# Performance work log

Hardware: AMD Instinct MI355X
Metric: run time of the kernel (lower is better)

The kernel has to match this reference:

```python
import jax, jax.numpy as jnp
import numpy as np
import math

B, S, H = 8, 1024, 1024
NH, DH = 16, 64  # MULTI_HEAD, HIDDEN_SIZE_HEAD


def setup_inputs() -> dict:
    key = jax.random.key(0)
    ks = jax.random.split(key, 12)
    scale = 0.02
    inp = {
        "v": jax.random.normal(ks[0], (B, S, H), jnp.float32),
        "k": jax.random.normal(ks[1], (B, S, H), jnp.float32),
        "q": jax.random.normal(ks[2], (B, S, H), jnp.float32),
        # True = masked position (masked_fill semantics)
        "mask": jax.random.bernoulli(ks[3], 0.1, (B, 1, 1, S)),
        "Wq": jax.random.normal(ks[4], (H, H), jnp.float32) * scale,
        "bq": jnp.zeros((H,), jnp.float32),
        "Wk": jax.random.normal(ks[5], (H, H), jnp.float32) * scale,
        "bk": jnp.zeros((H,), jnp.float32),
        "Wv": jax.random.normal(ks[6], (H, H), jnp.float32) * scale,
        "bv": jnp.zeros((H,), jnp.float32),
        "Wm": jax.random.normal(ks[7], (H, H), jnp.float32) * scale,
        "bm": jnp.zeros((H,), jnp.float32),
    }
    return inp


def _split_heads(x):
    # [B, S, H] -> [B, NH, S, DH]
    b, s, _ = x.shape
    return x.reshape(b, s, NH, DH).transpose(0, 2, 1, 3)


def reference(v, k, q, mask, Wq, bq, Wk, bk, Wv, bv, Wm, bm):
    # QKV projections (torch Linear: x @ W.T + b)
    qh = _split_heads(q @ Wq.T + bq)  # [B, NH, S, DH]
    kh = _split_heads(k @ Wk.T + bk)
    vh = _split_heads(v @ Wv.T + bv)

    scores = jnp.einsum("bhqd,bhkd->bhqk", qh, kh) / math.sqrt(DH)
    scores = jnp.where(mask, jnp.float32(-1e9), scores)
    att = jax.nn.softmax(scores, axis=-1)
    # dropout rate 0.0 (eval mode) -> identity
    ctx = jnp.einsum("bhqk,bhkd->bhqd", att, vh)  # [B, NH, S, DH]

    b = q.shape[0]
    merged = ctx.transpose(0, 2, 1, 3).reshape(b, -1, NH * DH)  # [B, S, H]
    return merged @ Wm.T + bm
```

## Files before the change

### kernel.cpp

```cpp
#include <hip/hip_runtime.h>
#include <hip/hip_bf16.h>

#define Bn 8
#define Sn 1024
#define Hn 1024
#define NHn 16
#define DHn 64
#define Mn (Bn * Sn)

typedef unsigned short u16;
typedef short bf16x8 __attribute__((ext_vector_type(8)));
typedef unsigned short u16x4 __attribute__((ext_vector_type(4)));
typedef float f32x4 __attribute__((ext_vector_type(4)));

__device__ __forceinline__ u16 f2bf(float x) {
  union { __hip_bfloat16 h; u16 u; } cv;
  cv.h = __float2bfloat16(x);
  return cv.u;
}

__device__ __forceinline__ void async_ld16(void* lds, const void* g) {
  __builtin_amdgcn_global_load_lds(
      (const __attribute__((address_space(1))) void*)g,
      (__attribute__((address_space(3))) void*)lds, 16, 0, 0);
}


__global__ __launch_bounds__(256) void sniff_k(const void* __restrict__ mask,
                                               int* __restrict__ flags) {
  __shared__ int viol;
  if (threadIdx.x == 0) viol = 0;
  __syncthreads();
  const unsigned* mw = (const unsigned*)mask;
  int vb = 0;
#pragma unroll
  for (int j = 0; j < 8; ++j) {
    unsigned v = mw[threadIdx.x * 8 + j];
    if (v > 1u) vb |= 1;
    if ((v & 0xFEFEFEFEu) != 0u) vb |= 2;
    if (!(v == 0u || v == 0x3F800000u)) vb |= 4;
    unsigned h0 = v & 0xFFFFu, h1 = v >> 16;
    if (!((h0 == 0u || h0 == 0x3F80u) && (h1 == 0u || h1 == 0x3F80u))) vb |= 8;
  }
  if (vb) atomicOr(&viol, vb);
  __syncthreads();
  if (threadIdx.x == 0) {
    int mt;
    if (!(viol & 1))      mt = 0;
    else if (!(viol & 2)) mt = 1;
    else if (!(viol & 4)) mt = 3;
    else if (!(viol & 8)) mt = 2;
    else                  mt = 0;
    flags[1] = mt;
  }
}

__global__ __launch_bounds__(256) void convert3(
    const float* __restrict__ a, const float* __restrict__ b,
    const float* __restrict__ c, u16* __restrict__ da,
    u16* __restrict__ db, u16* __restrict__ dc) {
  const int seg = blockIdx.x >> 12;
  const int bid = blockIdx.x & 4095;
  const float* s = seg == 0 ? a : seg == 1 ? b : c;
  u16* d        = seg == 0 ? da : seg == 1 ? db : dc;
  const int i = (bid * 256 + threadIdx.x) * 8;
  f32x4 lo = *(const f32x4*)(s + i);
  f32x4 hi = *(const f32x4*)(s + i + 4);
  bf16x8 o;
#pragma unroll
  for (int j = 0; j < 4; ++j) { o[j] = (short)f2bf(lo[j]); o[4 + j] = (short)f2bf(hi[j]); }
  *(bf16x8*)(d + i) = o;
}

__global__ __launch_bounds__(256) void convertW(
    const float* __restrict__ a, const float* __restrict__ b,
    const float* __restrict__ c, const float* __restrict__ e,
    u16* __restrict__ da, u16* __restrict__ db,
    u16* __restrict__ dc, u16* __restrict__ de) {
  const int seg = blockIdx.x >> 9;
  const int bid = blockIdx.x & 511;
  const float* s = seg == 0 ? a : seg == 1 ? b : seg == 2 ? c : e;
  u16* d        = seg == 0 ? da : seg == 1 ? db : seg == 2 ? dc : de;
  const int i = (bid * 256 + threadIdx.x) * 8;
  f32x4 lo = *(const f32x4*)(s + i);
  f32x4 hi = *(const f32x4*)(s + i + 4);
  bf16x8 o;
#pragma unroll
  for (int j = 0; j < 4; ++j) { o[j] = (short)f2bf(lo[j]); o[4 + j] = (short)f2bf(hi[j]); }
  *(bf16x8*)(d + i) = o;
}

template <int OMODE>
__device__ __forceinline__ void gemm_core(
    u16* As, u16* Bs, const u16* __restrict__ X, const u16* __restrict__ W,
    const float* __restrict__ bias, void* __restrict__ O, float scale)
{
  const int tid  = threadIdx.x;
  const int wave = tid >> 6;
  const int lane = tid & 63;
  const int ln   = lane & 15;
  const int quad = lane >> 4;
  const int bxr  = blockIdx.x;
  const int m0 = ((bxr & 7) * 8 + (bxr >> 3)) * 128;
  const int n0 = blockIdx.y * 128;
  const int wm = (wave & 1) * 64;
  const int wn = (wave >> 1) * 64;
  const int r8 = tid >> 3;
  const int cg = ((tid & 7) ^ (r8 & 7)) * 8;
  const int rsw = ln & 7;

  f32x4 acc[4][4] = {};

  auto STAGE = [&](int buf, int k0) {
    char* Ad = (char*)As + buf * 16384 + wave * 1024;
    char* Bd = (char*)Bs + buf * 16384 + wave * 1024;
#pragma unroll
    for (int j = 0; j < 4; ++j) {
      async_ld16(Ad + j * 4096, X + (size_t)(m0 + j * 32 + r8) * 1024 + k0 + cg);
      async_ld16(Bd + j * 4096, W + (size_t)(n0 + j * 32 + r8) * 1024 + k0 + cg);
    }
  };

  STAGE(0, 0);
  for (int step = 0; step < 16; ++step) {
    const int cur = step & 1;
    if (step < 15) {
      STAGE(cur ^ 1, (step + 1) * 64);
      asm volatile("s_waitcnt vmcnt(8)" ::: "memory");
    } else {
      asm volatile("s_waitcnt vmcnt(0)" ::: "memory");
    }
    asm volatile("s_barrier" ::: "memory");
    const char* Ab = (const char*)As + cur * 16384;
    const char* Bb = (const char*)Bs + cur * 16384;
#pragma unroll
    for (int s = 0; s < 2; ++s) {
      const int co = ((s * 4 + quad) ^ rsw) * 16;
      bf16x8 af[4], bfr[4];
#pragma unroll
      for (int t = 0; t < 4; ++t)
        af[t] = *(const bf16x8*)(Ab + (wm + t * 16 + ln) * 128 + co);
#pragma unroll
      for (int t = 0; t < 4; ++t)
        bfr[t] = *(const bf16x8*)(Bb + (wn + t * 16 + ln) * 128 + co);
#pragma unroll
      for (int i = 0; i < 4; ++i)
#pragma unroll
        for (int j = 0; j < 4; ++j)
          acc[i][j] = __builtin_amdgcn_mfma_f32_16x16x32_bf16(af[i], bfr[j], acc[i][j], 0, 0, 0);
    }
    asm volatile("s_barrier" ::: "memory");
  }

  if (OMODE == 2) {
    const int bb = m0 >> 10;
    const int sb = m0 & 1023;
#pragma unroll
    for (int j = 0; j < 4; ++j) {
      const int col = n0 + wn + j * 16 + ln;
      const float bv = bias[col];
#pragma unroll
      for (int i = 0; i < 4; ++i) {
        const int sl = sb + wm + i * 16 + quad * 4;
        u16x4 pk;
#pragma unroll
        for (int r = 0; r < 4; ++r) pk[r] = f2bf((acc[i][j][r] + bv) * scale);
        *(u16x4*)&((u16*)O)[((size_t)(bb * 1024 + col)) * 1024 + sl] = pk;
      }
    }
  } else {
#pragma unroll
    for (int j = 0; j < 4; ++j) {
      const int col = n0 + wn + j * 16 + ln;
      const float bv = bias[col];
#pragma unroll
      for (int i = 0; i < 4; ++i) {
        const int rowb = m0 + wm + i * 16 + quad * 4;
#pragma unroll
        for (int r = 0; r < 4; ++r) {
          const float val = (acc[i][j][r] + bv) * scale;
          const size_t idx = (size_t)(rowb + r) * 1024 + col;
          if (OMODE == 1) ((float*)O)[idx] = val;
          else            ((u16*)O)[idx]   = f2bf(val);
        }
      }
    }
  }
}

template <int OMODE>
__global__ __launch_bounds__(256, 2) void gemm_bt(
    const u16* __restrict__ X, const u16* __restrict__ W,
    const float* __restrict__ bias, void* __restrict__ O, float scale)
{
  __shared__ __attribute__((aligned(16))) u16 As[2 * 128 * 64];
  __shared__ __attribute__((aligned(16))) u16 Bs[2 * 128 * 64];
  gemm_core<OMODE>(As, Bs, X, W, bias, O, scale);
}

__global__ __launch_bounds__(256, 2) void gemm_qk(
    const u16* __restrict__ Xq, const u16* __restrict__ Wq,
    const float* __restrict__ bq, u16* __restrict__ Oq,
    const u16* __restrict__ Xk, const u16* __restrict__ Wk,
    const float* __restrict__ bk, u16* __restrict__ Ok)
{
  __shared__ __attribute__((aligned(16))) u16 As[2 * 128 * 64];
  __shared__ __attribute__((aligned(16))) u16 Bs[2 * 128 * 64];
  const int z = blockIdx.z;
  gemm_core<0>(As, Bs, z ? Xk : Xq, z ? Wk : Wq, z ? bk : bq,
               z ? (void*)Ok : (void*)Oq, z ? 1.0f : 0.125f);
}

__global__ __launch_bounds__(256, 3) void attn(
    const u16* __restrict__ Qb, const u16* __restrict__ Kb,
    const u16* __restrict__ Vbt, const void* __restrict__ mask,
    const int* __restrict__ flags, u16* __restrict__ Ctx)
{
  __shared__ __attribute__((aligned(16))) u16 Ks[128 * 64];
  __shared__ __attribute__((aligned(16))) u16 Vt[64 * 128];
  __shared__ __attribute__((aligned(16))) u16 Pl[4][16 * 128];
  __shared__ __attribute__((aligned(16))) float maskf[Sn];

  const int tid  = threadIdx.x;
  const int wave = tid >> 6;
  const int lane = tid & 63;
  const int ln   = lane & 15;
  const int quad = lane >> 4;
  const int bx  = blockIdx.x;
  const int x   = bx & 7;
  const int qt  = (bx >> 3) & 15;
  const int grp = bx >> 7;
  const int bh  = grp * 8 + x;
  const int b   = bh >> 4;
  const int h   = bh & 15;

  const int mt = flags[1];
  for (int i = tid; i < Sn; i += 256) {
    const int idx = b * Sn + i;
    int nz;
    if (mt == 0)      nz = ((const int*)mask)[idx] != 0;
    else if (mt == 1) nz = ((const signed char*)mask)[idx] != 0;
    else if (mt == 2) nz = ((const u16*)mask)[idx] != 0;
    else              nz = ((const unsigned*)mask)[idx] != 0;
    maskf[i] = nz ? -1e9f : 0.0f;
  }

  const size_t qoff = (size_t)(b * Sn + qt * 64 + wave * 16 + ln) * Hn + h * DHn;
  bf16x8 qf0 = *(const bf16x8*)&Qb[qoff + quad * 8];
  bf16x8 qf1 = *(const bf16x8*)&Qb[qoff + 32 + quad * 8];

  float mrun = -INFINITY, lrun = 0.0f;
  f32x4 acc[4] = {};

  const int kr = tid >> 1, kh = tid & 1;
  const int vd = tid >> 2, vs = tid & 3;
  char* pw  = (char*)Pl[wave];
  char* KsB = (char*)Ks;
  char* VtB = (char*)Vt;

  const int kwb = kr * 128 + kh * 64;
  const int ksw = (kr & 7) << 4;
  const int vwb = vd * 256 + vs * 64;
  const int vsw = (vd & 7) << 4;
  const int rsw = (ln & 7) << 4;
  const int pwb = ln * 256;
  const int psw = (ln & 7) << 4;

  const u16* kg = &Kb[(size_t)(b * Sn + kr) * Hn + h * DHn + kh * 32];
  const u16* vg = &Vbt[(size_t)(b * Sn + h * DHn + vd) * Sn + vs * 32];
  bf16x8 kreg[4], vreg[4];
#pragma unroll
  for (int j = 0; j < 4; ++j) kreg[j] = *(const bf16x8*)(kg + j * 8);
#pragma unroll
  for (int j = 0; j < 4; ++j) vreg[j] = *(const bf16x8*)(vg + j * 8);

  for (int t8 = 0; t8 < 8; ++t8) {
    const int kv0 = t8 * 128;
    __syncthreads();
#pragma unroll
    for (int j = 0; j < 4; ++j)
      *(bf16x8*)(KsB + ((kwb + j * 16) ^ ksw)) = kreg[j];
#pragma unroll
    for (int j = 0; j < 4; ++j)
      *(bf16x8*)(VtB + ((vwb + j * 16) ^ vsw)) = vreg[j];
    __syncthreads();

    if (t8 < 7) {
      const u16* kgn = kg + (size_t)(t8 + 1) * 128 * Hn;
      const u16* vgn = vg + (t8 + 1) * 128;
#pragma unroll
      for (int j = 0; j < 4; ++j) kreg[j] = *(const bf16x8*)(kgn + j * 8);
#pragma unroll
      for (int j = 0; j < 4; ++j) vreg[j] = *(const bf16x8*)(vgn + j * 8);
    }

    f32x4 sc[8];
#pragma unroll
    for (int t = 0; t < 8; ++t) {
      const int rb = (t * 16 + ln) * 128;
      bf16x8 kf0 = *(const bf16x8*)(KsB + ((rb + quad * 16) ^ rsw));
      bf16x8 kf1 = *(const bf16x8*)(KsB + ((rb + 64 + quad * 16) ^ rsw));
      f32x4 z = {};
      z = __builtin_amdgcn_mfma_f32_16x16x32_bf16(kf0, qf0, z, 0, 0, 0);
      z = __builtin_amdgcn_mfma_f32_16x16x32_bf16(kf1, qf1, z, 0, 0, 0);
      sc[t] = z;
    }
#pragma unroll
    for (int t = 0; t < 8; ++t) {
      const f32x4 mf4 = *(const f32x4*)&maskf[kv0 + t * 16 + quad * 4];
#pragma unroll
      for (int r = 0; r < 4; ++r) sc[t][r] += mf4[r];
    }

    f32x4 mm = sc[0];
#pragma unroll
    for (int t = 1; t < 8; ++t)
#pragma unroll
      for (int r = 0; r < 4; ++r) mm[r] = fmaxf(mm[r], sc[t][r]);
    float vmax = fmaxf(fmaxf(mm[0], mm[1]), fmaxf(mm[2], mm[3]));
    vmax = fmaxf(vmax, __shfl_xor(vmax, 16));
    vmax = fmaxf(vmax, __shfl_xor(vmax, 32));
    const float mnew = fmaxf(mrun, vmax);
    const float al = __expf(mrun - mnew);
    mrun = mnew;
    float ssum = 0.0f;
#pragma unroll
    for (int t = 0; t < 8; ++t)
#pragma unroll
      for (int r = 0; r < 4; ++r) {
        const float p = __expf(sc[t][r] - mnew);
        sc[t][r] = p;
        ssum += p;
      }
    ssum += __shfl_xor(ssum, 16);
    ssum += __shfl_xor(ssum, 32);
    lrun = lrun * al + ssum;

#pragma unroll
    for (int t = 0; t < 8; ++t) {
      u16x4 pk;
#pragma unroll
      for (int r = 0; r < 4; ++r) pk[r] = f2bf(sc[t][r]);
      *(u16x4*)(pw + ((pwb + t * 32 + quad * 8) ^ psw)) = pk;
    }

    float alr[4];
#pragma unroll
    for (int r = 0; r < 4; ++r) alr[r] = __shfl(al, quad * 4 + r);
#pragma unroll
    for (int dt = 0; dt < 4; ++dt)
#pragma unroll
      for (int r = 0; r < 4; ++r) acc[dt][r] *= alr[r];

    bf16x8 pa[4];
#pragma unroll
    for (int c = 0; c < 4; ++c)
      pa[c] = *(const bf16x8*)(pw + ((pwb + c * 64 + quad * 16) ^ psw));
#pragma unroll
    for (int dt = 0; dt < 4; ++dt) {
      const int vrb = (dt * 16 + ln) * 256;
#pragma unroll
      for (int c = 0; c < 4; ++c) {
        bf16x8 vb = *(const bf16x8*)(VtB + ((vrb + c * 64 + quad * 16) ^ rsw));
        acc[dt] = __builtin_amdgcn_mfma_f32_16x16x32_bf16(pa[c], vb, acc[dt], 0, 0, 0);
      }
    }
  }

  float lr[4];
#pragma unroll
  for (int r = 0; r < 4; ++r) lr[r] = __shfl(lrun, quad * 4 + r);
#pragma unroll
  for (int dt = 0; dt < 4; ++dt)
#pragma unroll
    for (int r = 0; r < 4; ++r) {
      const int s = qt * 64 + wave * 16 + quad * 4 + r;
      Ctx[(size_t)(b * Sn + s) * Hn + h * DHn + dt * 16 + ln] = f2bf(acc[dt][r] / lr[r]);
    }
}

extern "C" void kernel_launch(void* const* d_in, const int* in_sizes, int n_in,
                              void* d_out, int out_size, void* d_ws, size_t ws_size,
                              hipStream_t stream) {
  const float* v    = (const float*)d_in[0];
  const float* k    = (const float*)d_in[1];
  const float* q    = (const float*)d_in[2];
  const void*  mask = d_in[3];
  const float* Wq   = (const float*)d_in[4];
  const float* bq   = (const float*)d_in[5];
  const float* Wk   = (const float*)d_in[6];
  const float* bk   = (const float*)d_in[7];
  const float* Wv   = (const float*)d_in[8];
  const float* bv   = (const float*)d_in[9];
  const float* Wm   = (const float*)d_in[10];
  const float* bm   = (const float*)d_in[11];

  char* ws = (char*)d_ws;
  u16* qc  = (u16*)(ws);
  u16* kc  = (u16*)(ws + (16u << 20));
  u16* vc  = (u16*)(ws + (32u << 20));
  u16* Wqc = (u16*)(ws + (48u << 20));
  u16* Wkc = Wqc + (1u << 20);
  u16* Wvc = Wkc + (1u << 20);
  u16* Wmc = Wvc + (1u << 20);
  int* flags = (int*)(ws + (56u << 20));
  u16* Vbt = qc;
  u16* Cx  = kc;
  u16* Qb  = (u16*)d_out;
  u16* Kb  = Qb + (size_t)Mn * Hn;

  sniff_k<<<1, 256, 0, stream>>>(mask, flags);
  convert3<<<3 * 4096, 256, 0, stream>>>(q, k, v, qc, kc, vc);
  convertW<<<4 * 512, 256, 0, stream>>>(Wq, Wk, Wv, Wm, Wqc, Wkc, Wvc, Wmc);

  dim3 blk(256);
  gemm_qk<<<dim3(Mn / 128, Hn / 128, 2), blk, 0, stream>>>(
      qc, Wqc, bq, Qb, kc, Wkc, bk, Kb);
  dim3 grid(Mn / 128, Hn / 128);
  gemm_bt<2><<<grid, blk, 0, stream>>>(vc, Wvc, bv, Vbt, 1.0f);
  attn<<<dim3(Bn * NHn * (Sn / 64)), blk, 0, stream>>>(Qb, Kb, Vbt, mask, flags, Cx);
  gemm_bt<1><<<grid, blk, 0, stream>>>(Cx, Wmc, bm, d_out, 1.0f);
}
```

Before: 330.9 us.

## Process two 64-row query tiles per attention block to reuse K/V tiles

The attention kernel now handles 128 query rows per block: each wave keeps two 16-row query fragments (A and B) with separate online-softmax state and accumulators. Each K/V tile staged in LDS is reused for twice the query work, halving K/V global traffic and block count. The cost is higher register pressure (launch bounds lowered from 3 to 2 blocks per CU), a larger P buffer in LDS, and fewer blocks for load balancing.

```diff
diff --git a/kernel.cpp b/kernel.cpp
--- a/kernel.cpp
+++ b/kernel.cpp
@@ -24,7 +24,6 @@
       (const __attribute__((address_space(1))) void*)g,
       (__attribute__((address_space(3))) void*)lds, 16, 0, 0);
 }
-
 
 __global__ __launch_bounds__(256) void sniff_k(const void* __restrict__ mask,
                                                int* __restrict__ flags) {
@@ -211,14 +210,14 @@
                z ? (void*)Ok : (void*)Oq, z ? 1.0f : 0.125f);
 }
 
-__global__ __launch_bounds__(256, 3) void attn(
+__global__ __launch_bounds__(256, 2) void attn(
     const u16* __restrict__ Qb, const u16* __restrict__ Kb,
     const u16* __restrict__ Vbt, const void* __restrict__ mask,
     const int* __restrict__ flags, u16* __restrict__ Ctx)
 {
   __shared__ __attribute__((aligned(16))) u16 Ks[128 * 64];
   __shared__ __attribute__((aligned(16))) u16 Vt[64 * 128];
-  __shared__ __attribute__((aligned(16))) u16 Pl[4][16 * 128];
+  __shared__ __attribute__((aligned(16))) u16 Pl[4][32 * 128];
   __shared__ __attribute__((aligned(16))) float maskf[Sn];
 
   const int tid  = threadIdx.x;
@@ -228,8 +227,8 @@
   const int quad = lane >> 4;
   const int bx  = blockIdx.x;
   const int x   = bx & 7;
-  const int qt  = (bx >> 3) & 15;
-  const int grp = bx >> 7;
+  const int qt  = (bx >> 3) & 7;
+  const int grp = bx >> 6;
   const int bh  = grp * 8 + x;
   const int b   = bh >> 4;
   const int h   = bh & 15;
@@ -245,12 +244,16 @@
     maskf[i] = nz ? -1e9f : 0.0f;
   }
 
-  const size_t qoff = (size_t)(b * Sn + qt * 64 + wave * 16 + ln) * Hn + h * DHn;
-  bf16x8 qf0 = *(const bf16x8*)&Qb[qoff + quad * 8];
-  bf16x8 qf1 = *(const bf16x8*)&Qb[qoff + 32 + quad * 8];
-
-  float mrun = -INFINITY, lrun = 0.0f;
-  f32x4 acc[4] = {};
+  const size_t qoffA = (size_t)(b * Sn + qt * 128 + wave * 16 + ln) * Hn + h * DHn;
+  const size_t qoffB = qoffA + (size_t)64 * Hn;
+  bf16x8 qfA0 = *(const bf16x8*)&Qb[qoffA + quad * 8];
+  bf16x8 qfA1 = *(const bf16x8*)&Qb[qoffA + 32 + quad * 8];
+  bf16x8 qfB0 = *(const bf16x8*)&Qb[qoffB + quad * 8];
+  bf16x8 qfB1 = *(const bf16x8*)&Qb[qoffB + 32 + quad * 8];
+
+  float mrunA = -INFINITY, lrunA = 0.0f;
+  float mrunB = -INFINITY, lrunB = 0.0f;
+  f32x4 accA[4] = {}, accB[4] = {};
 
   const int kr = tid >> 1, kh = tid & 1;
   const int vd = tid >> 2, vs = tid & 3;
@@ -263,7 +266,8 @@
   const int vwb = vd * 256 + vs * 64;
   const int vsw = (vd & 7) << 4;
   const int rsw = (ln & 7) << 4;
-  const int pwb = ln * 256;
+  const int pwbA = ln * 256;
+  const int pwbB = (16 + ln) * 256;
   const int psw = (ln & 7) << 4;
 
   const u16* kg = &Kb[(size_t)(b * Sn + kr) * Hn + h * DHn + kh * 32];
@@ -294,88 +298,130 @@
       for (int j = 0; j < 4; ++j) vreg[j] = *(const bf16x8*)(vgn + j * 8);
     }
 
-    f32x4 sc[8];
+    f32x4 scA[8], scB[8];
 #pragma unroll
     for (int t = 0; t < 8; ++t) {
       const int rb = (t * 16 + ln) * 128;
       bf16x8 kf0 = *(const bf16x8*)(KsB + ((rb + quad * 16) ^ rsw));
       bf16x8 kf1 = *(const bf16x8*)(KsB + ((rb + 64 + quad * 16) ^ rsw));
-      f32x4 z = {};
-      z = __builtin_amdgcn_mfma_f32_16x16x32_bf16(kf0, qf0, z, 0, 0, 0);
-      z = __builtin_amdgcn_mfma_f32_16x16x32_bf16(kf1, qf1, z, 0, 0, 0);
-      sc[t] = z;
+      f32x4 zA = {}, zB = {};
+      zA = __builtin_amdgcn_mfma_f32_16x16x32_bf16(kf0, qfA0, zA, 0, 0, 0);
+      zA = __builtin_amdgcn_mfma_f32_16x16x32_bf16(kf1, qfA1, zA, 0, 0, 0);
+      zB = __builtin_amdgcn_mfma_f32_16x16x32_bf16(kf0, qfB0, zB, 0, 0, 0);
+      zB = __builtin_amdgcn_mfma_f32_16x16x32_bf16(kf1, qfB1, zB, 0, 0, 0);
+      scA[t] = zA;
+      scB[t] = zB;
     }
 #pragma unroll
     for (int t = 0; t < 8; ++t) {
       const f32x4 mf4 = *(const f32x4*)&maskf[kv0 + t * 16 + quad * 4];
 #pragma unroll
-      for (int r = 0; r < 4; ++r) sc[t][r] += mf4[r];
-    }
-
-    f32x4 mm = sc[0];
-#pragma unroll
-    for (int t = 1; t < 8; ++t)
-#pragma unroll
-      for (int r = 0; r < 4; ++r) mm[r] = fmaxf(mm[r], sc[t][r]);
-    float vmax = fmaxf(fmaxf(mm[0], mm[1]), fmaxf(mm[2], mm[3]));
-    vmax = fmaxf(vmax, __shfl_xor(vmax, 16));
-    vmax = fmaxf(vmax, __shfl_xor(vmax, 32));
-    const float mnew = fmaxf(mrun, vmax);
-    const float al = __expf(mrun - mnew);
-    mrun = mnew;
-    float ssum = 0.0f;
-#pragma unroll
-    for (int t = 0; t < 8; ++t)
-#pragma unroll
-      for (int r = 0; r < 4; ++r) {
-        const float p = __expf(sc[t][r] - mnew);
-        sc[t][r] = p;
-        ssum += p;
-      }
-    ssum += __shfl_xor(ssum, 16);
-    ssum += __shfl_xor(ssum, 32);
-    lrun = lrun * al + ssum;
+      for (int r = 0; r < 4; ++r) { scA[t][r] += mf4[r]; scB[t][r] += mf4[r]; }
+    }
+
+    float alA, alB;
+    {
+      f32x4 mm = scA[0];
+#pragma unroll
+      for (int t = 1; t < 8; ++t)
+#pragma unroll
+        for (int r = 0; r < 4; ++r) mm[r] = fmaxf(mm[r], scA[t][r]);
+      float vmax = fmaxf(fmaxf(mm[0], mm[1]), fmaxf(mm[2], mm[3]));
+      vmax = fmaxf(vmax, __shfl_xor(vmax, 16));
+      vmax = fmaxf(vmax, __shfl_xor(vmax, 32));
+      const float mnew = fmaxf(mrunA, vmax);
+      alA = __expf(mrunA - mnew);
+      mrunA = mnew;
+      float ssum = 0.0f;
+#pragma unroll
+      for (int t = 0; t < 8; ++t)
+#pragma unroll
+        for (int r = 0; r < 4; ++r) {
+          const float p = __expf(scA[t][r] - mnew);
+          scA[t][r] = p;
+          ssum += p;
+        }
+      ssum += __shfl_xor(ssum, 16);
+      ssum += __shfl_xor(ssum, 32);
+      lrunA = lrunA * alA + ssum;
+    }
+    {
+      f32x4 mm = scB[0];
+#pragma unroll
+      for (int t = 1; t < 8; ++t)
+#pragma unroll
+        for (int r = 0; r < 4; ++r) mm[r] = fmaxf(mm[r], scB[t][r]);
+      float vmax = fmaxf(fmaxf(mm[0], mm[1]), fmaxf(mm[2], mm[3]));
+      vmax = fmaxf(vmax, __shfl_xor(vmax, 16));
+      vmax = fmaxf(vmax, __shfl_xor(vmax, 32));
+      const float mnew = fmaxf(mrunB, vmax);
+      alB = __expf(mrunB - mnew);
+      mrunB = mnew;
+      float ssum = 0.0f;
+#pragma unroll
+      for (int t = 0; t < 8; ++t)
+#pragma unroll
+        for (int r = 0; r < 4; ++r) {
+          const float p = __expf(scB[t][r] - mnew);
+          scB[t][r] = p;
+          ssum += p;
+        }
+      ssum += __shfl_xor(ssum, 16);
+      ssum += __shfl_xor(ssum, 32);
+      lrunB = lrunB * alB + ssum;
+    }
 
 #pragma unroll
     for (int t = 0; t < 8; ++t) {
-      u16x4 pk;
-#pragma unroll
-      for (int r = 0; r < 4; ++r) pk[r] = f2bf(sc[t][r]);
-      *(u16x4*)(pw + ((pwb + t * 32 + quad * 8) ^ psw)) = pk;
-    }
-
-    float alr[4];
-#pragma unroll
-    for (int r = 0; r < 4; ++r) alr[r] = __shfl(al, quad * 4 + r);
+      u16x4 pkA, pkB;
+#pragma unroll
+      for (int r = 0; r < 4; ++r) { pkA[r] = f2bf(scA[t][r]); pkB[r] = f2bf(scB[t][r]); }
+      *(u16x4*)(pw + ((pwbA + t * 32 + quad * 8) ^ psw)) = pkA;
+      *(u16x4*)(pw + ((pwbB + t * 32 + quad * 8) ^ psw)) = pkB;
+    }
+
+    float alrA[4], alrB[4];
+#pragma unroll
+    for (int r = 0; r < 4; ++r) {
+      alrA[r] = __shfl(alA, quad * 4 + r);
+      alrB[r] = __shfl(alB, quad * 4 + r);
+    }
 #pragma unroll
     for (int dt = 0; dt < 4; ++dt)
 #pragma unroll
-      for (int r = 0; r < 4; ++r) acc[dt][r] *= alr[r];
-
-    bf16x8 pa[4];
-#pragma unroll
-    for (int c = 0; c < 4; ++c)
-      pa[c] = *(const bf16x8*)(pw + ((pwb + c * 64 + quad * 16) ^ psw));
+      for (int r = 0; r < 4; ++r) { accA[dt][r] *= alrA[r]; accB[dt][r] *= alrB[r]; }
+
+    bf16x8 paA[4], paB[4];
+#pragma unroll
+    for (int c = 0; c < 4; ++c) {
+      paA[c] = *(const bf16x8*)(pw + ((pwbA + c * 64 + quad * 16) ^ psw));
+      paB[c] = *(const bf16x8*)(pw + ((pwbB + c * 64 + quad * 16) ^ psw));
+    }
 #pragma unroll
     for (int dt = 0; dt < 4; ++dt) {
       const int vrb = (dt * 16 + ln) * 256;
 #pragma unroll
       for (int c = 0; c < 4; ++c) {
         bf16x8 vb = *(const bf16x8*)(VtB + ((vrb + c * 64 + quad * 16) ^ rsw));
-        acc[dt] = __builtin_amdgcn_mfma_f32_16x16x32_bf16(pa[c], vb, acc[dt], 0, 0, 0);
+        accA[dt] = __builtin_amdgcn_mfma_f32_16x16x32_bf16(paA[c], vb, accA[dt], 0, 0, 0);
+        accB[dt] = __builtin_amdgcn_mfma_f32_16x16x32_bf16(paB[c], vb, accB[dt], 0, 0, 0);
       }
     }
   }
 
-  float lr[4];
-#pragma unroll
-  for (int r = 0; r < 4; ++r) lr[r] = __shfl(lrun, quad * 4 + r);
+  float lrA[4], lrB[4];
+#pragma unroll
+  for (int r = 0; r < 4; ++r) {
+    lrA[r] = __shfl(lrunA, quad * 4 + r);
+    lrB[r] = __shfl(lrunB, quad * 4 + r);
+  }
 #pragma unroll
   for (int dt = 0; dt < 4; ++dt)
 #pragma unroll
     for (int r = 0; r < 4; ++r) {
-      const int s = qt * 64 + wave * 16 + quad * 4 + r;
-      Ctx[(size_t)(b * Sn + s) * Hn + h * DHn + dt * 16 + ln] = f2bf(acc[dt][r] / lr[r]);
+      const int sA = qt * 128 + wave * 16 + quad * 4 + r;
+      Ctx[(size_t)(b * Sn + sA) * Hn + h * DHn + dt * 16 + ln] = f2bf(accA[dt][r] / lrA[r]);
+      Ctx[(size_t)(b * Sn + sA + 64) * Hn + h * DHn + dt * 16 + ln] = f2bf(accB[dt][r] / lrB[r]);
     }
 }
 
@@ -418,6 +464,6 @@
       qc, Wqc, bq, Qb, kc, Wkc, bk, Kb);
   dim3 grid(Mn / 128, Hn / 128);
   gemm_bt<2><<<grid, blk, 0, stream>>>(vc, Wvc, bv, Vbt, 1.0f);
-  attn<<<dim3(Bn * NHn * (Sn / 64)), blk, 0, stream>>>(Qb, Kb, Vbt, mask, flags, Cx);
+  attn<<<dim3(Bn * NHn * (Sn / 128)), blk, 0, stream>>>(Qb, Kb, Vbt, mask, flags, Cx);
   gemm_bt<1><<<grid, blk, 0, stream>>>(Cx, Wmc, bm, d_out, 1.0f);
 }
```

Result: faster. 313.6 us (-5.2%).
